# Kernel optimization log

Hardware: AMD Instinct MI355X
Metric: run time of the kernel (lower is better)

## Reference

```python
import jax, jax.numpy as jnp
import numpy as np


def setup_inputs() -> dict:
    key = jax.random.key(0)
    ks = jax.random.split(key, 4)
    B, E, F, H, D = 64, 128, 1024, 512, 8
    s = jnp.float32(0.02)
    return {
        "x": jax.random.normal(ks[0], (B, E, F), dtype=jnp.float32),
        "W_ih": jax.random.normal(ks[1], (4 * H, F), dtype=jnp.float32) * s,
        "W_hh": jax.random.normal(ks[2], (4 * H, H), dtype=jnp.float32) * s,
        "b_ih": jnp.zeros((4 * H,), jnp.float32),
        "b_hh": jnp.zeros((4 * H,), jnp.float32),
        "W_cls": jax.random.normal(ks[3], (F, H), dtype=jnp.float32) * s,
        "b_cls": jnp.zeros((F,), jnp.float32),
        "dec_steps": 8,
    }


def reference(x, W_ih, W_hh, b_ih, b_hh, W_cls, b_cls, dec_steps):
    # feature_extractor is identity on precomputed features; dropout is eval-mode identity.
    # h_n/c_n are reset for every enc step, so all enc steps are independent:
    # flatten (B, E) -> one big batch and scan only over the sequential dec steps.
    B, E, F = x.shape
    H = W_hh.shape[1]
    out0 = x.reshape(B * E, F)
    h0 = jnp.zeros((B * E, H), x.dtype)
    c0 = jnp.zeros((B * E, H), x.dtype)
    bias = b_ih + b_hh  # [4H]

    def step(carry, _):
        h, c, out = carry
        gates = out @ W_ih.T + h @ W_hh.T + bias  # [BE, 4H]
        i, f, g, o = jnp.split(gates, 4, axis=-1)  # PyTorch LSTMCell gate order
        c = jax.nn.sigmoid(f) * c + jax.nn.sigmoid(i) * jnp.tanh(g)
        h = jax.nn.sigmoid(o) * jnp.tanh(c)
        out = h @ W_cls.T + b_cls  # [BE, F]
        return (h, c, out), out

    _, outs = jax.lax.scan(step, (h0, c0, out0), None, length=dec_steps)
    # outs: [D, BE, F] -> scores: [B, E, D, F]
    return outs.transpose(1, 0, 2).reshape(B, E, dec_steps, F)
```

## Files before the change

kernel.cpp:

```cpp
#include <hip/hip_runtime.h>
#include <hip/hip_bf16.h>

#define M_TOT 8192
#define FDIM  1024
#define HDIM  512
#define DSTEPS 8
#define BK 32

typedef __attribute__((ext_vector_type(8))) short short8;
typedef __attribute__((ext_vector_type(4))) float f32x4;

#define GLOAD_LDS16(gsrc, ldst)                                                        \
    __builtin_amdgcn_global_load_lds(                                                  \
        (__attribute__((address_space(1))) void*)(void*)(gsrc),                        \
        (__attribute__((address_space(3))) void*)(ldst), 16, 0, 0)

__device__ __forceinline__ unsigned short f2bf(float f) {
    unsigned u = __float_as_uint(f);
    return (unsigned short)((u + 0x7FFFu + ((u >> 16) & 1u)) >> 16);
}
__device__ __forceinline__ float sigm(float x) {
    return __builtin_amdgcn_rcpf(1.0f + __expf(-x));
}
__device__ __forceinline__ float tanh_(float x) {
    return 1.0f - 2.0f * __builtin_amdgcn_rcpf(1.0f + __expf(2.0f * x));
}

__global__ __launch_bounds__(256, 2) void gates_kernel(
    const __hip_bfloat16* __restrict__ Ab,
    const __hip_bfloat16* __restrict__ Wb,
    const float* __restrict__ bias,
    float* __restrict__ cbuf,
    __hip_bfloat16* __restrict__ hout,
    int ldk, int first)
{
    __shared__ __align__(16) __hip_bfloat16 sA[2][128 * BK];
    __shared__ __align__(16) __hip_bfloat16 sB[2][4 * 64 * BK];

    const int t    = threadIdx.x;
    const int wave = t >> 6;
    const int lane = t & 63;
    const int m0   = blockIdx.x * 128;
    const int j0   = blockIdx.y * 64;

    f32x4 acc[4][8];
    #pragma unroll
    for (int g = 0; g < 4; ++g)
        #pragma unroll
        for (int mi = 0; mi < 8; ++mi) acc[g][mi] = (f32x4)(0.0f);

    const int row_ld = t >> 2;
    const int kh     = t & 3;
    const int fr     = lane & 15;
    const int quad   = lane >> 4;

    auto STAGE = [&](int buf, int kc) {
        #pragma unroll
        for (int g = 0; g < 4; ++g) {
            GLOAD_LDS16(Wb + (size_t)(g * HDIM + j0 + row_ld) * ldk + kc * BK + kh * 8,
                        &sB[buf][(g * 256 + t) * 8]);
        }
        GLOAD_LDS16(Ab + (size_t)(m0 + row_ld) * ldk + kc * BK + kh * 8, &sA[buf][t * 8]);
        GLOAD_LDS16(Ab + (size_t)(m0 + 64 + row_ld) * ldk + kc * BK + kh * 8,
                    &sA[buf][2048 + t * 8]);
    };
    auto COMP = [&](int buf) {
        short8 bfrag[4];
        #pragma unroll
        for (int g = 0; g < 4; ++g)
            bfrag[g] = *(const short8*)&sB[buf][g * 64 * BK + (wave * 16 + fr) * BK + quad * 8];
        #pragma unroll
        for (int mi = 0; mi < 8; ++mi) {
            short8 afrag = *(const short8*)&sA[buf][(mi * 16 + fr) * BK + quad * 8];
            #pragma unroll
            for (int g = 0; g < 4; ++g)
                acc[g][mi] = __builtin_amdgcn_mfma_f32_16x16x32_bf16(afrag, bfrag[g], acc[g][mi], 0, 0, 0);
        }
    };

    const int nchunk = ldk / BK;
    STAGE(0, 0);
    for (int kc = 0; kc < nchunk; ++kc) {
        __syncthreads();
        if (kc + 1 < nchunk) STAGE((kc + 1) & 1, kc + 1);
        COMP(kc & 1);
    }

    const int col = j0 + wave * 16 + fr;
    const float bi = bias[col];
    const float bf = bias[HDIM + col];
    const float bg = bias[2 * HDIM + col];
    const float bo = bias[3 * HDIM + col];
    #pragma unroll
    for (int mi = 0; mi < 8; ++mi) {
        #pragma unroll
        for (int r = 0; r < 4; ++r) {
            const int row = m0 + mi * 16 + quad * 4 + r;
            const float iv = acc[0][mi][r] + bi;
            const float fv = acc[1][mi][r] + bf;
            const float gv = acc[2][mi][r] + bg;
            const float ov = acc[3][mi][r] + bo;
            const float cp = first ? 0.0f : cbuf[(size_t)row * HDIM + col];
            const float cn = sigm(fv) * cp + sigm(iv) * tanh_(gv);
            const float hn = sigm(ov) * tanh_(cn);
            cbuf[(size_t)row * HDIM + col] = cn;
            hout[(size_t)row * HDIM + col] = __hip_bfloat16(hn);
        }
    }
}

__global__ __launch_bounds__(256, 2) void cls_kernel(
    const __hip_bfloat16* __restrict__ hs,
    const __hip_bfloat16* __restrict__ Wclsb,
    const float* __restrict__ bcls,
    float* __restrict__ dout)
{
    __shared__ __align__(16) __hip_bfloat16 sA[2][128 * BK];
    __shared__ __align__(16) __hip_bfloat16 sB[2][4 * 64 * BK];

    const int t    = threadIdx.x;
    const int wave = t >> 6;
    const int lane = t & 63;
    const int m0   = blockIdx.x * 128;
    const int n0   = blockIdx.y * 256;
    const int tt   = blockIdx.x >> 6;

    f32x4 acc[4][8];
    #pragma unroll
    for (int g = 0; g < 4; ++g)
        #pragma unroll
        for (int mi = 0; mi < 8; ++mi) acc[g][mi] = (f32x4)(0.0f);

    const int row_ld = t >> 2;
    const int kh     = t & 3;
    const int fr     = lane & 15;
    const int quad   = lane >> 4;

    auto STAGE = [&](int buf, int kc) {
        #pragma unroll
        for (int g = 0; g < 4; ++g) {
            GLOAD_LDS16(Wclsb + (size_t)(n0 + g * 64 + row_ld) * HDIM + kc * BK + kh * 8,
                        &sB[buf][(g * 256 + t) * 8]);
        }
        GLOAD_LDS16(hs + (size_t)(m0 + row_ld) * HDIM + kc * BK + kh * 8, &sA[buf][t * 8]);
        GLOAD_LDS16(hs + (size_t)(m0 + 64 + row_ld) * HDIM + kc * BK + kh * 8,
                    &sA[buf][2048 + t * 8]);
    };
    auto COMP = [&](int buf) {
        short8 bfrag[4];
        #pragma unroll
        for (int g = 0; g < 4; ++g)
            bfrag[g] = *(const short8*)&sB[buf][g * 64 * BK + (wave * 16 + fr) * BK + quad * 8];
        #pragma unroll
        for (int mi = 0; mi < 8; ++mi) {
            short8 afrag = *(const short8*)&sA[buf][(mi * 16 + fr) * BK + quad * 8];
            #pragma unroll
            for (int g = 0; g < 4; ++g)
                acc[g][mi] = __builtin_amdgcn_mfma_f32_16x16x32_bf16(afrag, bfrag[g], acc[g][mi], 0, 0, 0);
        }
    };

    STAGE(0, 0);
    for (int kc = 0; kc < HDIM / BK; ++kc) {
        __syncthreads();
        if (kc + 1 < HDIM / BK) STAGE((kc + 1) & 1, kc + 1);
        COMP(kc & 1);
    }

    #pragma unroll
    for (int g = 0; g < 4; ++g) {
        const int col = n0 + g * 64 + wave * 16 + fr;
        const float bc = bcls[col];
        #pragma unroll
        for (int mi = 0; mi < 8; ++mi) {
            #pragma unroll
            for (int r = 0; r < 4; ++r) {
                const int row = m0 + mi * 16 + quad * 4 + r;
                const int m   = row & (M_TOT - 1);
                dout[(size_t)m * (DSTEPS * FDIM) + (size_t)tt * FDIM + col] =
                    acc[g][mi][r] + bc;
            }
        }
    }
}

__global__ __launch_bounds__(256) void fuse_gemm(
    const __hip_bfloat16* __restrict__ Wihb,
    const __hip_bfloat16* __restrict__ WclsT,
    const float* __restrict__ Whh,
    __hip_bfloat16* __restrict__ Wcombb)
{
    __shared__ __align__(16) __hip_bfloat16 sA[2][128 * BK];
    __shared__ __align__(16) __hip_bfloat16 sB[2][128 * BK];

    const int t    = threadIdx.x;
    const int wave = t >> 6;
    const int lane = t & 63;
    const int wr   = wave >> 1;
    const int wc   = wave & 1;
    const int m0   = blockIdx.x * 128;
    const int n0   = blockIdx.y * 128;

    f32x4 acc[4][4];
    #pragma unroll
    for (int ni = 0; ni < 4; ++ni)
        #pragma unroll
        for (int mi = 0; mi < 4; ++mi) acc[ni][mi] = (f32x4)(0.0f);

    const int row_ld = t >> 2;
    const int kh     = t & 3;
    const int fr     = lane & 15;
    const int quad   = lane >> 4;

    auto STAGE = [&](int buf, int kc) {
        GLOAD_LDS16(Wihb + (size_t)(m0 + row_ld) * FDIM + kc * BK + kh * 8, &sA[buf][t * 8]);
        GLOAD_LDS16(Wihb + (size_t)(m0 + 64 + row_ld) * FDIM + kc * BK + kh * 8,
                    &sA[buf][2048 + t * 8]);
        GLOAD_LDS16(WclsT + (size_t)(n0 + row_ld) * FDIM + kc * BK + kh * 8, &sB[buf][t * 8]);
        GLOAD_LDS16(WclsT + (size_t)(n0 + 64 + row_ld) * FDIM + kc * BK + kh * 8,
                    &sB[buf][2048 + t * 8]);
    };
    auto COMP = [&](int buf) {
        short8 afrag[4], bfrag[4];
        #pragma unroll
        for (int i = 0; i < 4; ++i) {
            afrag[i] = *(const short8*)&sA[buf][(wr * 64 + i * 16 + fr) * BK + quad * 8];
            bfrag[i] = *(const short8*)&sB[buf][(wc * 64 + i * 16 + fr) * BK + quad * 8];
        }
        #pragma unroll
        for (int ni = 0; ni < 4; ++ni)
            #pragma unroll
            for (int mi = 0; mi < 4; ++mi)
                acc[ni][mi] = __builtin_amdgcn_mfma_f32_16x16x32_bf16(afrag[mi], bfrag[ni], acc[ni][mi], 0, 0, 0);
    };

    STAGE(0, 0);
    for (int kc = 0; kc < FDIM / BK; ++kc) {
        __syncthreads();
        if (kc + 1 < FDIM / BK) STAGE((kc + 1) & 1, kc + 1);
        COMP(kc & 1);
    }

    #pragma unroll
    for (int ni = 0; ni < 4; ++ni) {
        const int col = n0 + wc * 64 + ni * 16 + fr;
        #pragma unroll
        for (int mi = 0; mi < 4; ++mi) {
            #pragma unroll
            for (int r = 0; r < 4; ++r) {
                const int row = m0 + wr * 64 + mi * 16 + quad * 4 + r;
                const float v = acc[ni][mi][r] + Whh[(size_t)row * HDIM + col];
                Wcombb[(size_t)row * HDIM + col] = __hip_bfloat16(v);
            }
        }
    }
}

__global__ void transpose_cls(const float* __restrict__ Wcls,
                              __hip_bfloat16* __restrict__ WclsT) {
    __shared__ float tile[32][33];
    const int f0 = blockIdx.x * 32;
    const int h0 = blockIdx.y * 32;
    const int tx = threadIdx.x, ty = threadIdx.y;
    #pragma unroll
    for (int k = 0; k < 4; ++k)
        tile[ty + 8 * k][tx] = Wcls[(size_t)(f0 + ty + 8 * k) * HDIM + h0 + tx];
    __syncthreads();
    #pragma unroll
    for (int k = 0; k < 4; ++k)
        WclsT[(size_t)(h0 + ty + 8 * k) * FDIM + f0 + tx] =
            __hip_bfloat16(tile[tx][ty + 8 * k]);
}

__global__ void fuse_bias(const float* __restrict__ bih, const float* __restrict__ bhh,
                          const float* __restrict__ Wih, const float* __restrict__ bcls,
                          float* __restrict__ bias0, float* __restrict__ biasF) {
    const int r   = blockIdx.x;
    const int tid = threadIdx.x;
    float s = 0.0f;
    for (int k = tid; k < FDIM; k += 256) s += Wih[(size_t)r * FDIM + k] * bcls[k];
    #pragma unroll
    for (int off = 32; off; off >>= 1) s += __shfl_down(s, off, 64);
    __shared__ float red[4];
    if ((tid & 63) == 0) red[tid >> 6] = s;
    __syncthreads();
    if (tid == 0) {
        const float b = bih[r] + bhh[r];
        bias0[r] = b;
        biasF[r] = b + red[0] + red[1] + red[2] + red[3];
    }
}

__global__ void cvt_bf16(const float* __restrict__ src, __hip_bfloat16* __restrict__ dst, int n8) {
    int i = blockIdx.x * blockDim.x + threadIdx.x;
    if (i < n8) {
        const float4 a = ((const float4*)src)[2 * i];
        const float4 b = ((const float4*)src)[2 * i + 1];
        short8 v;
        v[0] = (short)f2bf(a.x); v[1] = (short)f2bf(a.y);
        v[2] = (short)f2bf(a.z); v[3] = (short)f2bf(a.w);
        v[4] = (short)f2bf(b.x); v[5] = (short)f2bf(b.y);
        v[6] = (short)f2bf(b.z); v[7] = (short)f2bf(b.w);
        ((short8*)dst)[i] = v;
    }
}

extern "C" void kernel_launch(void* const* d_in, const int* in_sizes, int n_in,
                              void* d_out, int out_size, void* d_ws, size_t ws_size,
                              hipStream_t stream) {
    const float* x    = (const float*)d_in[0];
    const float* Wih  = (const float*)d_in[1];
    const float* Whh  = (const float*)d_in[2];
    const float* bih  = (const float*)d_in[3];
    const float* bhh  = (const float*)d_in[4];
    const float* Wcls = (const float*)d_in[5];
    const float* bcls = (const float*)d_in[6];
    float* out = (float*)d_out;

    char* ws = (char*)d_ws;
    __hip_bfloat16* Wihb   = (__hip_bfloat16*)(ws);
    __hip_bfloat16* Wclsb  = (__hip_bfloat16*)(ws + (4ull  << 20));
    __hip_bfloat16* WclsT  = (__hip_bfloat16*)(ws + (5ull  << 20));
    __hip_bfloat16* Wcombb = (__hip_bfloat16*)(ws + (6ull  << 20));
    float*          bias0  = (float*)         (ws + (8ull  << 20));
    float*          biasF  = (float*)         (ws + (8ull  << 20) + 32768);
    __hip_bfloat16* xb     = (__hip_bfloat16*)(ws + (9ull  << 20));
    float*          cbuf   = (float*)         (ws + (25ull << 20));
    __hip_bfloat16* hs     = (__hip_bfloat16*)(ws + (41ull << 20));

    cvt_bf16<<<dim3(2048 * 1024 / 8 / 256), dim3(256), 0, stream>>>(Wih,  Wihb,  2048 * 1024 / 8);
    cvt_bf16<<<dim3(1024 * 512  / 8 / 256), dim3(256), 0, stream>>>(Wcls, Wclsb, 1024 * 512  / 8);
    cvt_bf16<<<dim3(8192 * 1024 / 8 / 256), dim3(256), 0, stream>>>(x,    xb,    8192 * 1024 / 8);
    transpose_cls<<<dim3(FDIM / 32, HDIM / 32), dim3(32, 8), 0, stream>>>(Wcls, WclsT);
    fuse_gemm<<<dim3(2048 / 128, HDIM / 128), dim3(256), 0, stream>>>(Wihb, WclsT, Whh, Wcombb);
    fuse_bias<<<dim3(2048), dim3(256), 0, stream>>>(bih, bhh, Wih, bcls, bias0, biasF);

    const size_t hstride = (size_t)M_TOT * HDIM;
    gates_kernel<<<dim3(M_TOT / 128, HDIM / 64), dim3(256), 0, stream>>>(
        xb, Wihb, bias0, cbuf, hs, FDIM, 1);
    for (int t = 1; t < DSTEPS; ++t) {
        gates_kernel<<<dim3(M_TOT / 128, HDIM / 64), dim3(256), 0, stream>>>(
            hs + (size_t)(t - 1) * hstride, Wcombb, biasF, cbuf, hs + (size_t)t * hstride,
            HDIM, 0);
    }
    cls_kernel<<<dim3(DSTEPS * M_TOT / 128, FDIM / 256), dim3(256), 0, stream>>>(
        hs, Wclsb, bcls, out);
}
```

Baseline: 711.5 us.

## Fuse all LSTM decode steps into one persistent kernel with LDS-resident state

New measurement: 1.110 ms. 1.56x slower.

```diff
diff --git a/kernel.cpp b/kernel.cpp
--- a/kernel.cpp
+++ b/kernel.cpp
@@ -26,86 +26,135 @@
     return 1.0f - 2.0f * __builtin_amdgcn_rcpf(1.0f + __expf(2.0f * x));
 }
 
-__global__ __launch_bounds__(256, 2) void gates_kernel(
-    const __hip_bfloat16* __restrict__ Ab,
-    const __hip_bfloat16* __restrict__ Wb,
-    const float* __restrict__ bias,
-    float* __restrict__ cbuf,
-    __hip_bfloat16* __restrict__ hout,
-    int ldk, int first)
+template <int LDK, int ROWE, int NCH>
+__device__ __forceinline__ void kloop(const __hip_bfloat16* __restrict__ W,
+                                      const __hip_bfloat16 (&sX)[32 * 1024],
+                                      f32x4 (&acc)[4][4][2],
+                                      int colw, int fr, int quad) {
+    #pragma unroll 2
+    for (int kc = 0; kc < NCH; ++kc) {
+        short8 af[2];
+        #pragma unroll
+        for (int mi = 0; mi < 2; ++mi) {
+            const int row = mi * 16 + fr;
+            af[mi] = *(const short8*)&sX[row * ROWE + ((kc * 4 + quad) ^ (fr & 7)) * 8];
+        }
+        #pragma unroll
+        for (int cg = 0; cg < 4; ++cg) {
+            const __hip_bfloat16* wp =
+                W + (size_t)(colw + cg * 16 + fr) * LDK + kc * 32 + quad * 8;
+            #pragma unroll
+            for (int g = 0; g < 4; ++g) {
+                const short8 b8 = *(const short8*)(wp + (size_t)g * (512 * LDK));
+                #pragma unroll
+                for (int mi = 0; mi < 2; ++mi)
+                    acc[g][cg][mi] = __builtin_amdgcn_mfma_f32_16x16x32_bf16(
+                        af[mi], b8, acc[g][cg][mi], 0, 0, 0);
+            }
+        }
+    }
+}
+
+__device__ __forceinline__ void pointwise(f32x4 (&acc)[4][4][2], f32x4 (&c)[4][2],
+                                          const float (&bi)[4], const float (&bf)[4],
+                                          const float (&bg)[4], const float (&bo)[4],
+                                          __hip_bfloat16 (&sX)[32 * 1024],
+                                          __hip_bfloat16* __restrict__ hs_t,
+                                          int m0, int colw, int fr, int quad) {
+    __syncthreads();
+    #pragma unroll
+    for (int cg = 0; cg < 4; ++cg) {
+        const int col = colw + cg * 16 + fr;
+        #pragma unroll
+        for (int mi = 0; mi < 2; ++mi) {
+            #pragma unroll
+            for (int r = 0; r < 4; ++r) {
+                const int row = mi * 16 + quad * 4 + r;
+                const float iv = acc[0][cg][mi][r] + bi[cg];
+                const float fv = acc[1][cg][mi][r] + bf[cg];
+                const float gv = acc[2][cg][mi][r] + bg[cg];
+                const float ov = acc[3][cg][mi][r] + bo[cg];
+                const float cn = sigm(fv) * c[cg][mi][r] + sigm(iv) * tanh_(gv);
+                const float hn = sigm(ov) * tanh_(cn);
+                c[cg][mi][r]   = cn;
+                const __hip_bfloat16 hb = __hip_bfloat16(hn);
+                sX[row * 512 + ((((col >> 3) ^ (row & 7)) << 3) + (col & 7))] = hb;
+                hs_t[(size_t)(m0 + row) * HDIM + col] = hb;
+            }
+        }
+    }
+    __syncthreads();
+}
+
+#define ZACC()                                                                         \
+    _Pragma("unroll") for (int g = 0; g < 4; ++g)                                      \
+        _Pragma("unroll") for (int cg = 0; cg < 4; ++cg)                               \
+            _Pragma("unroll") for (int mi = 0; mi < 2; ++mi) acc[g][cg][mi] = (f32x4)(0.0f);
+
+__global__ __launch_bounds__(512, 2) void lstm_chain(
+    const __hip_bfloat16* __restrict__ xb,
+    const __hip_bfloat16* __restrict__ Wihb,
+    const __hip_bfloat16* __restrict__ Wcombb,
+    const float* __restrict__ bias0,
+    const float* __restrict__ biasF,
+    __hip_bfloat16* __restrict__ hs)
 {
-    __shared__ __align__(16) __hip_bfloat16 sA[2][128 * BK];
-    __shared__ __align__(16) __hip_bfloat16 sB[2][4 * 64 * BK];
-
-    const int t    = threadIdx.x;
-    const int wave = t >> 6;
-    const int lane = t & 63;
-    const int m0   = blockIdx.x * 128;
-    const int j0   = blockIdx.y * 64;
-
-    f32x4 acc[4][8];
-    #pragma unroll
-    for (int g = 0; g < 4; ++g)
-        #pragma unroll
-        for (int mi = 0; mi < 8; ++mi) acc[g][mi] = (f32x4)(0.0f);
-
-    const int row_ld = t >> 2;
-    const int kh     = t & 3;
-    const int fr     = lane & 15;
-    const int quad   = lane >> 4;
-
-    auto STAGE = [&](int buf, int kc) {
-        #pragma unroll
-        for (int g = 0; g < 4; ++g) {
-            GLOAD_LDS16(Wb + (size_t)(g * HDIM + j0 + row_ld) * ldk + kc * BK + kh * 8,
-                        &sB[buf][(g * 256 + t) * 8]);
-        }
-        GLOAD_LDS16(Ab + (size_t)(m0 + row_ld) * ldk + kc * BK + kh * 8, &sA[buf][t * 8]);
-        GLOAD_LDS16(Ab + (size_t)(m0 + 64 + row_ld) * ldk + kc * BK + kh * 8,
-                    &sA[buf][2048 + t * 8]);
-    };
-    auto COMP = [&](int buf) {
-        short8 bfrag[4];
-        #pragma unroll
-        for (int g = 0; g < 4; ++g)
-            bfrag[g] = *(const short8*)&sB[buf][g * 64 * BK + (wave * 16 + fr) * BK + quad * 8];
-        #pragma unroll
-        for (int mi = 0; mi < 8; ++mi) {
-            short8 afrag = *(const short8*)&sA[buf][(mi * 16 + fr) * BK + quad * 8];
-            #pragma unroll
-            for (int g = 0; g < 4; ++g)
-                acc[g][mi] = __builtin_amdgcn_mfma_f32_16x16x32_bf16(afrag, bfrag[g], acc[g][mi], 0, 0, 0);
-        }
-    };
-
-    const int nchunk = ldk / BK;
-    STAGE(0, 0);
-    for (int kc = 0; kc < nchunk; ++kc) {
-        __syncthreads();
-        if (kc + 1 < nchunk) STAGE((kc + 1) & 1, kc + 1);
-        COMP(kc & 1);
-    }
-
-    const int col = j0 + wave * 16 + fr;
-    const float bi = bias[col];
-    const float bf = bias[HDIM + col];
-    const float bg = bias[2 * HDIM + col];
-    const float bo = bias[3 * HDIM + col];
-    #pragma unroll
-    for (int mi = 0; mi < 8; ++mi) {
-        #pragma unroll
-        for (int r = 0; r < 4; ++r) {
-            const int row = m0 + mi * 16 + quad * 4 + r;
-            const float iv = acc[0][mi][r] + bi;
-            const float fv = acc[1][mi][r] + bf;
-            const float gv = acc[2][mi][r] + bg;
-            const float ov = acc[3][mi][r] + bo;
-            const float cp = first ? 0.0f : cbuf[(size_t)row * HDIM + col];
-            const float cn = sigm(fv) * cp + sigm(iv) * tanh_(gv);
-            const float hn = sigm(ov) * tanh_(cn);
-            cbuf[(size_t)row * HDIM + col] = cn;
-            hout[(size_t)row * HDIM + col] = __hip_bfloat16(hn);
-        }
+    __shared__ __align__(16) __hip_bfloat16 sX[32 * 1024];
+
+    const int tid  = threadIdx.x;
+    const int wave = tid >> 6;
+    const int lane = tid & 63;
+    const int fr   = lane & 15;
+    const int quad = lane >> 4;
+    const int m0   = blockIdx.x * 32;
+    const int colw = wave * 64;
+
+    #pragma unroll
+    for (int j = 0; j < 8; ++j) {
+        const int n   = (wave * 8 + j) * 64 + lane;
+        const int row = n >> 7;
+        const int su  = (n & 127) ^ (row & 7);
+        GLOAD_LDS16(xb + (size_t)(m0 + row) * FDIM + su * 8,
+                    &sX[(wave * 8 + j) * 512]);
+    }
+
+    f32x4 acc[4][4][2];
+    f32x4 c[4][2];
+    #pragma unroll
+    for (int cg = 0; cg < 4; ++cg)
+        #pragma unroll
+        for (int mi = 0; mi < 2; ++mi) c[cg][mi] = (f32x4)(0.0f);
+
+    float bi[4], bf[4], bg[4], bo[4];
+    #pragma unroll
+    for (int cg = 0; cg < 4; ++cg) {
+        const int col = colw + cg * 16 + fr;
+        bi[cg] = bias0[col];
+        bf[cg] = bias0[HDIM + col];
+        bg[cg] = bias0[2 * HDIM + col];
+        bo[cg] = bias0[3 * HDIM + col];
+    }
+
+    __syncthreads();
+
+    ZACC();
+    kloop<1024, 1024, 32>(Wihb, sX, acc, colw, fr, quad);
+    pointwise(acc, c, bi, bf, bg, bo, sX, hs, m0, colw, fr, quad);
+
+    #pragma unroll
+    for (int cg = 0; cg < 4; ++cg) {
+        const int col = colw + cg * 16 + fr;
+        bi[cg] = biasF[col];
+        bf[cg] = biasF[HDIM + col];
+        bg[cg] = biasF[2 * HDIM + col];
+        bo[cg] = biasF[3 * HDIM + col];
+    }
+
+    for (int t = 1; t < DSTEPS; ++t) {
+        ZACC();
+        kloop<512, 512, 16>(Wcombb, sX, acc, colw, fr, quad);
+        pointwise(acc, c, bi, bf, bg, bo, sX, hs + (size_t)t * M_TOT * HDIM,
+                  m0, colw, fr, quad);
     }
 }
 
@@ -325,8 +374,7 @@
     float*          bias0  = (float*)         (ws + (8ull  << 20));
     float*          biasF  = (float*)         (ws + (8ull  << 20) + 32768);
     __hip_bfloat16* xb     = (__hip_bfloat16*)(ws + (9ull  << 20));
-    float*          cbuf   = (float*)         (ws + (25ull << 20));
-    __hip_bfloat16* hs     = (__hip_bfloat16*)(ws + (41ull << 20));
+    __hip_bfloat16* hs     = (__hip_bfloat16*)(ws + (25ull << 20));
 
     cvt_bf16<<<dim3(2048 * 1024 / 8 / 256), dim3(256), 0, stream>>>(Wih,  Wihb,  2048 * 1024 / 8);
     cvt_bf16<<<dim3(1024 * 512  / 8 / 256), dim3(256), 0, stream>>>(Wcls, Wclsb, 1024 * 512  / 8);
@@ -335,14 +383,9 @@
     fuse_gemm<<<dim3(2048 / 128, HDIM / 128), dim3(256), 0, stream>>>(Wihb, WclsT, Whh, Wcombb);
     fuse_bias<<<dim3(2048), dim3(256), 0, stream>>>(bih, bhh, Wih, bcls, bias0, biasF);
 
-    const size_t hstride = (size_t)M_TOT * HDIM;
-    gates_kernel<<<dim3(M_TOT / 128, HDIM / 64), dim3(256), 0, stream>>>(
-        xb, Wihb, bias0, cbuf, hs, FDIM, 1);
-    for (int t = 1; t < DSTEPS; ++t) {
-        gates_kernel<<<dim3(M_TOT / 128, HDIM / 64), dim3(256), 0, stream>>>(
-            hs + (size_t)(t - 1) * hstride, Wcombb, biasF, cbuf, hs + (size_t)t * hstride,
-            HDIM, 0);
-    }
+    lstm_chain<<<dim3(M_TOT / 32), dim3(512), 0, stream>>>(
+        xb, Wihb, Wcombb, bias0, biasF, hs);
+
     cls_kernel<<<dim3(DSTEPS * M_TOT / 128, FDIM / 256), dim3(256), 0, stream>>>(
         hs, Wclsb, bcls, out);
 }
```
